# Performance work log

Measured on AMD Instinct MI355X. Metric: run time of the kernel, lower is better.

## Reference

```python
import jax, jax.numpy as jnp
import numpy as np
import math

B, S, D = 1, 2048, 2048
NQ, NKV = 32, 8
HD = D // NQ            # 64
NREP = NQ // NKV        # 4
EPS = 1e-6


def _rope_tables(seq_len, head_dim, theta=10000.0):
    half = head_dim // 2
    inv_freq = 1.0 / (theta ** (np.arange(0, half, dtype=np.float32) / half))
    t = np.arange(seq_len, dtype=np.float32)
    freqs = np.outer(t, inv_freq)  # [S, half]
    return jnp.asarray(np.cos(freqs)), jnp.asarray(np.sin(freqs))


def _rmsnorm(x, g, eps=EPS):
    denom = jnp.sqrt(jnp.mean(x * x, axis=-1, keepdims=True) + eps)
    return x / denom * g


def _rope(x, cos, sin):
    # x: [B, S, H, HD]; cos/sin: [S, HD//2]
    half = x.shape[-1] // 2
    x1, x2 = x[..., :half], x[..., half:]
    c = cos[None, :, None, :]
    s = sin[None, :, None, :]
    return jnp.concatenate([x1 * c - x2 * s, x1 * s + x2 * c], axis=-1)


def setup_inputs() -> dict:
    key = jax.random.key(0)
    ks = jax.random.split(key, 6)
    scale = 1.0 / math.sqrt(D)
    x = jax.random.normal(ks[0], (B, S, D), dtype=jnp.float32)
    Wq = jax.random.normal(ks[1], (D, NQ * HD), dtype=jnp.float32) * scale
    Wk = jax.random.normal(ks[2], (D, NKV * HD), dtype=jnp.float32) * scale
    Wv = jax.random.normal(ks[3], (D, NKV * HD), dtype=jnp.float32) * scale
    Wo = jax.random.normal(ks[4], (NQ * HD, D), dtype=jnp.float32) * scale
    g_q = jnp.ones((HD,), dtype=jnp.float32)
    g_k = jnp.ones((HD,), dtype=jnp.float32)
    cos, sin = _rope_tables(S, HD)
    return {"x": x, "cos": cos, "sin": sin, "g_q": g_q, "g_k": g_k,
            "Wq": Wq, "Wk": Wk, "Wv": Wv, "Wo": Wo}


def reference(x, cos, sin, g_q, g_k, Wq, Wk, Wv, Wo):
    bs, seq, _ = x.shape
    Q = (x @ Wq).reshape(bs, seq, NQ, HD)
    K = (x @ Wk).reshape(bs, seq, NKV, HD)
    V = (x @ Wv).reshape(bs, seq, NKV, HD)
    Q = _rope(_rmsnorm(Q, g_q), cos, sin)
    K = _rope(_rmsnorm(K, g_k), cos, sin)
    # GQA: repeat_interleave KV heads to match Q heads
    K = jnp.repeat(K, NREP, axis=2)  # [B,S,NQ,HD]
    V = jnp.repeat(V, NREP, axis=2)
    # scores: [B, H, S, S]
    scores = jnp.einsum('bshd,bthd->bhst', Q, K) / math.sqrt(HD)
    mask = jnp.triu(jnp.ones((seq, seq), dtype=bool), k=1)
    scores = jnp.where(mask, -jnp.inf, scores)
    attn = jax.nn.softmax(scores, axis=-1)
    out = jnp.einsum('bhst,bthd->bshd', attn, V).reshape(bs, seq, NQ * HD)
    return out @ Wo
```

## Files before the change

### kernel.cpp

```cpp
#include <hip/hip_runtime.h>
#include <hip/hip_bf16.h>
#include <math.h>

#define S 2048
#define D 2048
#define NQ 32
#define NKV 8
#define HD 64
#define HALF 32
#define NREP 4
#define QKV_N 3072
#define KCOL 2048
#define VCOL 2560

typedef unsigned short ushort_t;
typedef __attribute__((ext_vector_type(8))) short bf16x8;
typedef __attribute__((ext_vector_type(4))) float f32x4;
typedef float f4 __attribute__((ext_vector_type(4)));

__device__ __forceinline__ ushort_t f2bf(float f) {
    __hip_bfloat16 h = __float2bfloat16(f);
    return *reinterpret_cast<ushort_t*>(&h);
}
__device__ __forceinline__ float bf2f(ushort_t u) {
    __hip_bfloat16 h = *reinterpret_cast<__hip_bfloat16*>(&u);
    return __bfloat162float(h);
}

__device__ __forceinline__ void load_lds16(const ushort_t* g, ushort_t* l) {
    __builtin_amdgcn_global_load_lds(
        (const __attribute__((address_space(1))) unsigned int*)g,
        (__attribute__((address_space(3))) unsigned int*)l,
        16, 0, 0);
}

__global__ __launch_bounds__(256) void convert_bf16(const float* __restrict__ src,
                                                    ushort_t* __restrict__ dst, int n) {
    int i = (blockIdx.x * 256 + threadIdx.x) * 4;
    if (i + 3 < n) {
        f4 v = *(const f4*)&src[i];
        dst[i + 0] = f2bf(v[0]);
        dst[i + 1] = f2bf(v[1]);
        dst[i + 2] = f2bf(v[2]);
        dst[i + 3] = f2bf(v[3]);
    }
}

__global__ __launch_bounds__(256) void zero_f32(f4* __restrict__ p, int n4) {
    int i = blockIdx.x * 256 + threadIdx.x;
    if (i < n4) p[i] = (f4){0.f, 0.f, 0.f, 0.f};
}

__global__ __launch_bounds__(256) void transpose_w(const float* __restrict__ src,
                                                   ushort_t* __restrict__ dst,
                                                   int Kdim, int N, int pitch, int row_off) {
    __shared__ float tile[32][33];
    const int n0 = blockIdx.x * 32, k0 = blockIdx.y * 32;
    const int tx = threadIdx.x & 31, ty = threadIdx.x >> 5;
    #pragma unroll
    for (int i = 0; i < 32; i += 8)
        tile[ty + i][tx] = src[(size_t)(k0 + ty + i) * N + (n0 + tx)];
    __syncthreads();
    #pragma unroll
    for (int i = 0; i < 32; i += 8)
        dst[(size_t)(row_off + n0 + ty + i) * pitch + (k0 + tx)] = f2bf(tile[tx][ty + i]);
}

__global__ __launch_bounds__(256) void transpose_v(const ushort_t* __restrict__ src,
                                                   ushort_t* __restrict__ dst) {
    __shared__ ushort_t tile[32][33];
    const int s0 = blockIdx.x * 32, d0 = blockIdx.y * 32;
    const int tx = threadIdx.x & 31, ty = threadIdx.x >> 5;
    #pragma unroll
    for (int i = 0; i < 32; i += 8)
        tile[ty + i][tx] = src[(size_t)(s0 + ty + i) * QKV_N + VCOL + d0 + tx];
    __syncthreads();
    #pragma unroll
    for (int i = 0; i < 32; i += 8)
        dst[(size_t)(d0 + ty + i) * S + s0 + tx] = tile[tx][ty + i];
}

template <typename OutT>
__global__ __launch_bounds__(256) void gemm_bt64(const ushort_t* __restrict__ A,
                                                 const ushort_t* __restrict__ BT,
                                                 OutT* __restrict__ C,
                                                 int M, int N, int Kdim) {
    __shared__ ushort_t As[64][32];
    __shared__ ushort_t Bs[128][32];
    const int tid = threadIdx.x;
    const int w = tid >> 6, lane = tid & 63;
    const int r16 = lane & 15, quad = lane >> 4;
    const int wm = (w >> 1) * 32, wn = (w & 1) * 64;
    const int bm = blockIdx.y * 64, bn = blockIdx.x * 128;
    const int sr = lane >> 2;
    const int sc8 = (lane & 3) * 8;

    f32x4 acc[2][4];
    #pragma unroll
    for (int r = 0; r < 2; ++r)
        #pragma unroll
        for (int c = 0; c < 4; ++c) acc[r][c] = (f32x4){0.f, 0.f, 0.f, 0.f};

    for (int k0 = 0; k0 < Kdim; k0 += 32) {
        __syncthreads();
        load_lds16(A + (size_t)(bm + w * 16 + sr) * Kdim + k0 + sc8, &As[w * 16][0]);
        #pragma unroll
        for (int i = 0; i < 2; ++i)
            load_lds16(BT + (size_t)(bn + w * 32 + i * 16 + sr) * Kdim + k0 + sc8,
                       &Bs[w * 32 + i * 16][0]);
        __syncthreads();

        bf16x8 af[2], bfr[4];
        #pragma unroll
        for (int r = 0; r < 2; ++r) af[r]  = *(const bf16x8*)&As[wm + 16 * r + r16][quad * 8];
        #pragma unroll
        for (int c = 0; c < 4; ++c) bfr[c] = *(const bf16x8*)&Bs[wn + 16 * c + r16][quad * 8];
        #pragma unroll
        for (int r = 0; r < 2; ++r)
            #pragma unroll
            for (int c = 0; c < 4; ++c)
                acc[r][c] = __builtin_amdgcn_mfma_f32_16x16x32_bf16(af[r], bfr[c], acc[r][c], 0, 0, 0);
    }

    #pragma unroll
    for (int r = 0; r < 2; ++r)
        #pragma unroll
        for (int c = 0; c < 4; ++c)
            #pragma unroll
            for (int reg = 0; reg < 4; ++reg) {
                int row = bm + wm + 16 * r + quad * 4 + reg;
                int col = bn + wn + 16 * c + r16;
                float v = acc[r][c][reg];
                if constexpr (sizeof(OutT) == 2) C[(size_t)row * N + col] = (OutT)f2bf(v);
                else                             C[(size_t)row * N + col] = (OutT)v;
            }
}

__global__ __launch_bounds__(256) void rmsnorm_rope_b(ushort_t* __restrict__ QKV,
                                                      const float* __restrict__ gq,
                                                      const float* __restrict__ gk,
                                                      const float* __restrict__ cosT,
                                                      const float* __restrict__ sinT) {
    const int s = blockIdx.x;
    const int w = threadIdx.x >> 6;
    const int hh = blockIdx.y * 4 + w;
    const int d = threadIdx.x & 63;
    const float* g;
    int col;
    if (hh < NQ) { g = gq; col = hh * HD; }
    else         { g = gk; col = KCOL + (hh - NQ) * HD; }

    ushort_t* xp = QKV + (size_t)s * QKV_N + col;
    float v = bf2f(xp[d]);
    float ss = v * v;
    #pragma unroll
    for (int off = 32; off > 0; off >>= 1) ss += __shfl_down(ss, off);
    ss = __shfl(ss, 0);
    float inv = rsqrtf(ss * (1.0f / HD) + 1e-6f);
    float xn = v * inv * g[d];

    float other = __shfl(xn, d ^ 32);
    float c = cosT[(size_t)s * HALF + (d & 31)];
    float sn = sinT[(size_t)s * HALF + (d & 31)];
    float outv = (d < HALF) ? (xn * c - other * sn) : (other * sn + xn * c);
    xp[d] = f2bf(outv);
}

__global__ __launch_bounds__(256) void flash_attn_mfma(const ushort_t* __restrict__ QKV,
                                                       const ushort_t* __restrict__ VTg,
                                                       ushort_t* __restrict__ O,
                                                       float* __restrict__ AccBuf,
                                                       float* __restrict__ AccL) {
    __shared__ ushort_t Ks[2][64][64];
    __shared__ ushort_t Vt[2][64][64];
    __shared__ ushort_t Ps[4][16][72];

    const int bx = blockIdx.x;
    int qt, tb, te;
    bool atom;
    if (bx < 16) { qt = 16 + bx; tb = 0; te = 16; atom = true; }
    else         { qt = 47 - bx; atom = (qt >= 16); tb = atom ? 16 : 0; te = qt + 1; }

    const int q0 = qt * 64;
    const int h  = blockIdx.y;
    const int kvh = h >> 2;
    const int tid = threadIdx.x;
    const int w = tid >> 6, lane = tid & 63;
    const int r16 = lane & 15, quad = lane >> 4;
    const int kcol = KCOL + kvh * HD;
    const int vtrow0 = kvh * HD;
    const int rsub = lane >> 3;
    const int jlog = (lane & 7) ^ rsub;
    const int rx = r16 & 7;

    const ushort_t* qrow = QKV + (size_t)(q0 + 16 * w + r16) * QKV_N + h * HD;
    bf16x8 qf0, qf1;
    {
        bf16x8 r0 = *(const bf16x8*)(qrow + quad * 8);
        bf16x8 r1 = *(const bf16x8*)(qrow + quad * 8 + 32);
        #pragma unroll
        for (int j = 0; j < 8; ++j) {
            qf0[j] = (short)f2bf(bf2f((ushort_t)r0[j]) * 0.18033688f);
            qf1[j] = (short)f2bf(bf2f((ushort_t)r1[j]) * 0.18033688f);
        }
    }

    bf16x8 onesf;
    {
        ushort_t ov = (r16 == 0) ? (ushort_t)0x3F80 : (ushort_t)0;
        #pragma unroll
        for (int j = 0; j < 8; ++j) onesf[j] = (short)ov;
    }

    f32x4 accO[4];
    f32x4 accL = (f32x4){0.f, 0.f, 0.f, 0.f};
    #pragma unroll
    for (int c = 0; c < 4; ++c) accO[c] = (f32x4){0.f, 0.f, 0.f, 0.f};

    auto stage = [&](int b, int t0) {
        #pragma unroll
        for (int i = 0; i < 2; ++i) {
            int base = w * 16 + i * 8;
            int row = base + rsub;
            load_lds16(QKV + (size_t)(t0 + row) * QKV_N + kcol + jlog * 8, &Ks[b][base][0]);
            load_lds16(VTg + (size_t)(vtrow0 + row) * S + t0 + jlog * 8, &Vt[b][base][0]);
        }
    };

    stage(tb & 1, tb * 64);

    for (int t = tb; t < te; ++t) {
        __syncthreads();
        if (t + 1 < te) stage((t + 1) & 1, (t + 1) * 64);

        const ushort_t (*K_)[64] = Ks[t & 1];
        const ushort_t (*V_)[64] = Vt[t & 1];
        const bool diag = (t == qt);

        f32x4 sc[4];
        #pragma unroll
        for (int c = 0; c < 4; ++c) {
            bf16x8 kf0 = *(const bf16x8*)&K_[16 * c + r16][(quad ^ rx) * 8];
            bf16x8 kf1 = *(const bf16x8*)&K_[16 * c + r16][((quad + 4) ^ rx) * 8];
            f32x4 z = (f32x4){0.f, 0.f, 0.f, 0.f};
            z = __builtin_amdgcn_mfma_f32_16x16x32_bf16(qf0, kf0, z, 0, 0, 0);
            z = __builtin_amdgcn_mfma_f32_16x16x32_bf16(qf1, kf1, z, 0, 0, 0);
            sc[c] = z;
        }

        #pragma unroll
        for (int c = 0; c < 4; ++c)
            #pragma unroll
            for (int reg = 0; reg < 4; ++reg) {
                float v = sc[c][reg];
                if (diag && (16 * c + r16 > 16 * w + quad * 4 + reg)) v = -INFINITY;
                float p = exp2f(v);
                Ps[w][quad * 4 + reg][16 * c + r16] = f2bf(p);
            }

        bf16x8 pf0 = *(const bf16x8*)&Ps[w][r16][quad * 8];
        bf16x8 pf1 = *(const bf16x8*)&Ps[w][r16][quad * 8 + 32];

        accL = __builtin_amdgcn_mfma_f32_16x16x32_bf16(pf0, onesf, accL, 0, 0, 0);
        accL = __builtin_amdgcn_mfma_f32_16x16x32_bf16(pf1, onesf, accL, 0, 0, 0);

        #pragma unroll
        for (int c = 0; c < 4; ++c) {
            bf16x8 vf0 = *(const bf16x8*)&V_[16 * c + r16][(quad ^ rx) * 8];
            bf16x8 vf1 = *(const bf16x8*)&V_[16 * c + r16][((quad + 4) ^ rx) * 8];
            accO[c] = __builtin_amdgcn_mfma_f32_16x16x32_bf16(pf0, vf0, accO[c], 0, 0, 0);
            accO[c] = __builtin_amdgcn_mfma_f32_16x16x32_bf16(pf1, vf1, accO[c], 0, 0, 0);
        }
    }

    if (!atom) {
        #pragma unroll
        for (int reg = 0; reg < 4; ++reg) {
            float l = __shfl(accL[reg], lane & 48);
            float invl = 1.0f / l;
            int row = q0 + 16 * w + quad * 4 + reg;
            ushort_t* op = O + (size_t)row * D + h * HD;
            #pragma unroll
            for (int c = 0; c < 4; ++c)
                op[16 * c + r16] = f2bf(accO[c][reg] * invl);
        }
    } else {
        const int pair = (qt - 16) * 32 + h;
        float* ab = AccBuf + (size_t)pair * 4096;
        #pragma unroll
        for (int reg = 0; reg < 4; ++reg) {
            int row = 16 * w + quad * 4 + reg;
            #pragma unroll
            for (int c = 0; c < 4; ++c)
                atomicAdd(&ab[row * 64 + 16 * c + r16], accO[c][reg]);
        }
        if (r16 == 0) {
            #pragma unroll
            for (int reg = 0; reg < 4; ++reg)
                atomicAdd(&AccL[pair * 64 + 16 * w + quad * 4 + reg], accL[reg]);
        }
    }
}

__global__ __launch_bounds__(256) void normalize_o(const float* __restrict__ AccBuf,
                                                   const float* __restrict__ AccL,
                                                   ushort_t* __restrict__ O) {
    const int pair = blockIdx.x;
    const int qt = 16 + (pair >> 5);
    const int h  = pair & 31;
    const float* ab = AccBuf + (size_t)pair * 4096;
    const float* lp = AccL + pair * 64;
    for (int i = threadIdx.x; i < 4096; i += 256) {
        int row = i >> 6, d = i & 63;
        O[(size_t)(qt * 64 + row) * D + h * HD + d] = f2bf(ab[i] / lp[row]);
    }
}

extern "C" void kernel_launch(void* const* d_in, const int* in_sizes, int n_in,
                              void* d_out, int out_size, void* d_ws, size_t ws_size,
                              hipStream_t stream) {
    const float* x    = (const float*)d_in[0];
    const float* cosT = (const float*)d_in[1];
    const float* sinT = (const float*)d_in[2];
    const float* g_q  = (const float*)d_in[3];
    const float* g_k  = (const float*)d_in[4];
    const float* Wq   = (const float*)d_in[5];
    const float* Wk   = (const float*)d_in[6];
    const float* Wv   = (const float*)d_in[7];
    const float* Wo   = (const float*)d_in[8];
    float* out = (float*)d_out;

    char* base = (char*)d_ws;
    ushort_t* Xb     = (ushort_t*)base;
    ushort_t* WqkvT  = (ushort_t*)(base + 8388608);
    ushort_t* QKVb   = (ushort_t*)(base + 20971520);
    float*    AccBuf = (float*)(base + 8388608);
    ushort_t* WoT    = (ushort_t*)(base + 8388608);
    ushort_t* VTg    = (ushort_t*)(base + 16777216);
    float*    AccL   = (float*)(base + 18874368);
    ushort_t* Ob     = Xb;

    convert_bf16<<<(S * D) / 1024, 256, 0, stream>>>(x, Xb, S * D);
    transpose_w<<<dim3(2048 / 32, 2048 / 32), 256, 0, stream>>>(Wq, WqkvT, 2048, 2048, 2048, 0);
    transpose_w<<<dim3(512 / 32, 2048 / 32), 256, 0, stream>>>(Wk, WqkvT, 2048, 512, 2048, 2048);
    transpose_w<<<dim3(512 / 32, 2048 / 32), 256, 0, stream>>>(Wv, WqkvT, 2048, 512, 2048, 2560);
    gemm_bt64<ushort_t><<<dim3(QKV_N / 128, S / 64), 256, 0, stream>>>(Xb, WqkvT, QKVb, S, QKV_N, D);
    rmsnorm_rope_b<<<dim3(S, 10), 256, 0, stream>>>(QKVb, g_q, g_k, cosT, sinT);
    transpose_v<<<dim3(S / 32, 512 / 32), 256, 0, stream>>>(QKVb, VTg);
    zero_f32<<<(2097152 / 4 + 255) / 256, 256, 0, stream>>>((f4*)AccBuf, 2097152 / 4);
    zero_f32<<<(32768 / 4 + 255) / 256, 256, 0, stream>>>((f4*)AccL, 32768 / 4);
    flash_attn_mfma<<<dim3(48, NQ), 256, 0, stream>>>(QKVb, VTg, Ob, AccBuf, AccL);
    normalize_o<<<512, 256, 0, stream>>>(AccBuf, AccL, Ob);
    transpose_w<<<dim3(2048 / 32, 2048 / 32), 256, 0, stream>>>(Wo, WoT, 2048, 2048, 2048, 0);
    gemm_bt64<float><<<dim3(D / 128, S / 64), 256, 0, stream>>>(Ob, WoT, out, S, D, D);
}
```

Before: 282.1 us.

## Merge prep kernels, retile GEMM to 64x64 with K=64, shrink attention KV tile

Fuses the x conversion and Q/K/V weight transposes into one launch. RMSNorm+RoPE, the V transpose and the Wo transpose now share a single launch, and the two zeroing kernels become one. The GEMM moves to 64x64 output tiles with a K step of 64 and XOR-swizzled LDS. Attention stages 32-key tiles instead of 64, and the accumulation buffer is moved into the output allocation. The aim is to cut launch overhead and raise block counts, at the cost of smaller per-iteration MFMA work and more loop iterations.

```diff
diff --git a/kernel.cpp b/kernel.cpp
--- a/kernel.cpp
+++ b/kernel.cpp
@@ -34,28 +34,29 @@
         16, 0, 0);
 }
 
-__global__ __launch_bounds__(256) void convert_bf16(const float* __restrict__ src,
-                                                    ushort_t* __restrict__ dst, int n) {
-    int i = (blockIdx.x * 256 + threadIdx.x) * 4;
-    if (i + 3 < n) {
-        f4 v = *(const f4*)&src[i];
-        dst[i + 0] = f2bf(v[0]);
-        dst[i + 1] = f2bf(v[1]);
-        dst[i + 2] = f2bf(v[2]);
-        dst[i + 3] = f2bf(v[3]);
-    }
-}
-
-__global__ __launch_bounds__(256) void zero_f32(f4* __restrict__ p, int n4) {
-    int i = blockIdx.x * 256 + threadIdx.x;
-    if (i < n4) p[i] = (f4){0.f, 0.f, 0.f, 0.f};
-}
-
-__global__ __launch_bounds__(256) void transpose_w(const float* __restrict__ src,
-                                                   ushort_t* __restrict__ dst,
-                                                   int Kdim, int N, int pitch, int row_off) {
+__global__ __launch_bounds__(256) void prep_all(const float* __restrict__ x,
+                                                ushort_t* __restrict__ Xb,
+                                                const float* __restrict__ Wq,
+                                                const float* __restrict__ Wk,
+                                                const float* __restrict__ Wv,
+                                                ushort_t* __restrict__ WqkvT) {
     __shared__ float tile[32][33];
-    const int n0 = blockIdx.x * 32, k0 = blockIdx.y * 32;
+    const int b = blockIdx.x;
+    if (b < 4096) {
+        int i = (b * 256 + threadIdx.x) * 4;
+        f4 v = *(const f4*)&x[i];
+        Xb[i + 0] = f2bf(v[0]);
+        Xb[i + 1] = f2bf(v[1]);
+        Xb[i + 2] = f2bf(v[2]);
+        Xb[i + 3] = f2bf(v[3]);
+        return;
+    }
+    const float* src; int N, row_off, t;
+    if (b < 8192)      { src = Wq; N = 2048; row_off = 0;    t = b - 4096; }
+    else if (b < 9216) { src = Wk; N = 512;  row_off = 2048; t = b - 8192; }
+    else               { src = Wv; N = 512;  row_off = 2560; t = b - 9216; }
+    const int ntn = N / 32;
+    const int n0 = (t % ntn) * 32, k0 = (t / ntn) * 32;
     const int tx = threadIdx.x & 31, ty = threadIdx.x >> 5;
     #pragma unroll
     for (int i = 0; i < 32; i += 8)
@@ -63,69 +64,62 @@
     __syncthreads();
     #pragma unroll
     for (int i = 0; i < 32; i += 8)
-        dst[(size_t)(row_off + n0 + ty + i) * pitch + (k0 + tx)] = f2bf(tile[tx][ty + i]);
-}
-
-__global__ __launch_bounds__(256) void transpose_v(const ushort_t* __restrict__ src,
-                                                   ushort_t* __restrict__ dst) {
-    __shared__ ushort_t tile[32][33];
-    const int s0 = blockIdx.x * 32, d0 = blockIdx.y * 32;
-    const int tx = threadIdx.x & 31, ty = threadIdx.x >> 5;
-    #pragma unroll
-    for (int i = 0; i < 32; i += 8)
-        tile[ty + i][tx] = src[(size_t)(s0 + ty + i) * QKV_N + VCOL + d0 + tx];
-    __syncthreads();
-    #pragma unroll
-    for (int i = 0; i < 32; i += 8)
-        dst[(size_t)(d0 + ty + i) * S + s0 + tx] = tile[tx][ty + i];
+        WqkvT[(size_t)(row_off + n0 + ty + i) * 2048 + (k0 + tx)] = f2bf(tile[tx][ty + i]);
 }
 
 template <typename OutT>
-__global__ __launch_bounds__(256) void gemm_bt64(const ushort_t* __restrict__ A,
-                                                 const ushort_t* __restrict__ BT,
-                                                 OutT* __restrict__ C,
-                                                 int M, int N, int Kdim) {
-    __shared__ ushort_t As[64][32];
-    __shared__ ushort_t Bs[128][32];
+__global__ __launch_bounds__(256) void gemm64(const ushort_t* __restrict__ A,
+                                              const ushort_t* __restrict__ BT,
+                                              OutT* __restrict__ C,
+                                              int M, int N, int Kdim) {
+    __shared__ ushort_t As[64][64];
+    __shared__ ushort_t Bs[64][64];
     const int tid = threadIdx.x;
     const int w = tid >> 6, lane = tid & 63;
     const int r16 = lane & 15, quad = lane >> 4;
-    const int wm = (w >> 1) * 32, wn = (w & 1) * 64;
-    const int bm = blockIdx.y * 64, bn = blockIdx.x * 128;
-    const int sr = lane >> 2;
-    const int sc8 = (lane & 3) * 8;
-
-    f32x4 acc[2][4];
+    const int wm = (w >> 1) * 32, wn = (w & 1) * 32;
+    const int bm = blockIdx.y * 64, bn = blockIdx.x * 64;
+    const int srow = lane >> 3;
+    const int jl = (lane & 7) ^ srow;
+    const int rx = r16 & 7;
+
+    f32x4 acc[2][2];
     #pragma unroll
     for (int r = 0; r < 2; ++r)
         #pragma unroll
-        for (int c = 0; c < 4; ++c) acc[r][c] = (f32x4){0.f, 0.f, 0.f, 0.f};
-
-    for (int k0 = 0; k0 < Kdim; k0 += 32) {
+        for (int c = 0; c < 2; ++c) acc[r][c] = (f32x4){0.f, 0.f, 0.f, 0.f};
+
+    for (int k0 = 0; k0 < Kdim; k0 += 64) {
         __syncthreads();
-        load_lds16(A + (size_t)(bm + w * 16 + sr) * Kdim + k0 + sc8, &As[w * 16][0]);
-        #pragma unroll
-        for (int i = 0; i < 2; ++i)
-            load_lds16(BT + (size_t)(bn + w * 32 + i * 16 + sr) * Kdim + k0 + sc8,
-                       &Bs[w * 32 + i * 16][0]);
+        #pragma unroll
+        for (int i = 0; i < 2; ++i) {
+            int rbase = w * 16 + i * 8;
+            load_lds16(A  + (size_t)(bm + rbase + srow) * Kdim + k0 + jl * 8, &As[rbase][0]);
+            load_lds16(BT + (size_t)(bn + rbase + srow) * Kdim + k0 + jl * 8, &Bs[rbase][0]);
+        }
         __syncthreads();
 
-        bf16x8 af[2], bfr[4];
-        #pragma unroll
-        for (int r = 0; r < 2; ++r) af[r]  = *(const bf16x8*)&As[wm + 16 * r + r16][quad * 8];
-        #pragma unroll
-        for (int c = 0; c < 4; ++c) bfr[c] = *(const bf16x8*)&Bs[wn + 16 * c + r16][quad * 8];
-        #pragma unroll
-        for (int r = 0; r < 2; ++r)
-            #pragma unroll
-            for (int c = 0; c < 4; ++c)
-                acc[r][c] = __builtin_amdgcn_mfma_f32_16x16x32_bf16(af[r], bfr[c], acc[r][c], 0, 0, 0);
+        #pragma unroll
+        for (int h = 0; h < 2; ++h) {
+            bf16x8 af[2], bfr[2];
+            #pragma unroll
+            for (int r = 0; r < 2; ++r)
+                af[r]  = *(const bf16x8*)&As[wm + 16 * r + r16][((quad + 4 * h) ^ rx) * 8];
+            #pragma unroll
+            for (int c = 0; c < 2; ++c)
+                bfr[c] = *(const bf16x8*)&Bs[wn + 16 * c + r16][((quad + 4 * h) ^ rx) * 8];
+            #pragma unroll
+            for (int r = 0; r < 2; ++r)
+                #pragma unroll
+                for (int c = 0; c < 2; ++c)
+                    acc[r][c] = __builtin_amdgcn_mfma_f32_16x16x32_bf16(af[r], bfr[c], acc[r][c], 0, 0, 0);
+        }
     }
 
     #pragma unroll
     for (int r = 0; r < 2; ++r)
         #pragma unroll
-        for (int c = 0; c < 4; ++c)
+        for (int c = 0; c < 2; ++c)
             #pragma unroll
             for (int reg = 0; reg < 4; ++reg) {
                 int row = bm + wm + 16 * r + quad * 4 + reg;
@@ -136,34 +130,73 @@
             }
 }
 
-__global__ __launch_bounds__(256) void rmsnorm_rope_b(ushort_t* __restrict__ QKV,
-                                                      const float* __restrict__ gq,
-                                                      const float* __restrict__ gk,
-                                                      const float* __restrict__ cosT,
-                                                      const float* __restrict__ sinT) {
-    const int s = blockIdx.x;
-    const int w = threadIdx.x >> 6;
-    const int hh = blockIdx.y * 4 + w;
-    const int d = threadIdx.x & 63;
-    const float* g;
-    int col;
-    if (hh < NQ) { g = gq; col = hh * HD; }
-    else         { g = gk; col = KCOL + (hh - NQ) * HD; }
-
-    ushort_t* xp = QKV + (size_t)s * QKV_N + col;
-    float v = bf2f(xp[d]);
-    float ss = v * v;
-    #pragma unroll
-    for (int off = 32; off > 0; off >>= 1) ss += __shfl_down(ss, off);
-    ss = __shfl(ss, 0);
-    float inv = rsqrtf(ss * (1.0f / HD) + 1e-6f);
-    float xn = v * inv * g[d];
-
-    float other = __shfl(xn, d ^ 32);
-    float c = cosT[(size_t)s * HALF + (d & 31)];
-    float sn = sinT[(size_t)s * HALF + (d & 31)];
-    float outv = (d < HALF) ? (xn * c - other * sn) : (other * sn + xn * c);
-    xp[d] = f2bf(outv);
+__global__ __launch_bounds__(256) void rms_rope_vwo(ushort_t* __restrict__ QKV,
+                                                    const float* __restrict__ gq,
+                                                    const float* __restrict__ gk,
+                                                    const float* __restrict__ cosT,
+                                                    const float* __restrict__ sinT,
+                                                    ushort_t* __restrict__ VTg,
+                                                    const float* __restrict__ Wo,
+                                                    ushort_t* __restrict__ WoT) {
+    const int y = blockIdx.y, xb = blockIdx.x;
+    if (y < 10) {
+        const int s = xb;
+        const int w = threadIdx.x >> 6;
+        const int hh = y * 4 + w;
+        const int d = threadIdx.x & 63;
+        const float* g;
+        int col;
+        if (hh < NQ) { g = gq; col = hh * HD; }
+        else         { g = gk; col = KCOL + (hh - NQ) * HD; }
+        ushort_t* xp = QKV + (size_t)s * QKV_N + col;
+        float v = bf2f(xp[d]);
+        float ss = v * v;
+        #pragma unroll
+        for (int off = 32; off > 0; off >>= 1) ss += __shfl_down(ss, off);
+        ss = __shfl(ss, 0);
+        float inv = rsqrtf(ss * (1.0f / HD) + 1e-6f);
+        float xn = v * inv * g[d];
+        float other = __shfl(xn, d ^ 32);
+        float c = cosT[(size_t)s * HALF + (d & 31)];
+        float sn = sinT[(size_t)s * HALF + (d & 31)];
+        float outv = (d < HALF) ? (xn * c - other * sn) : (other * sn + xn * c);
+        xp[d] = f2bf(outv);
+        return;
+    }
+    const int tx = threadIdx.x & 31, ty = threadIdx.x >> 5;
+    if (y == 10 && xb < 1024) {
+        __shared__ ushort_t vt[32][33];
+        const int s0 = (xb & 63) * 32, d0 = (xb >> 6) * 32;
+        #pragma unroll
+        for (int i = 0; i < 32; i += 8)
+            vt[ty + i][tx] = QKV[(size_t)(s0 + ty + i) * QKV_N + VCOL + d0 + tx];
+        __syncthreads();
+        #pragma unroll
+        for (int i = 0; i < 32; i += 8)
+            VTg[(size_t)(d0 + ty + i) * S + s0 + tx] = vt[tx][ty + i];
+        return;
+    }
+    int idx;
+    if (y == 10)      idx = xb - 1024;
+    else if (y == 11) idx = 1024 + xb;
+    else              idx = 3072 + xb;
+    if (idx < 0 || idx >= 4096) return;
+    __shared__ float wt[32][33];
+    const int n0 = (idx & 63) * 32, k0 = (idx >> 6) * 32;
+    #pragma unroll
+    for (int i = 0; i < 32; i += 8)
+        wt[ty + i][tx] = Wo[(size_t)(k0 + ty + i) * 2048 + (n0 + tx)];
+    __syncthreads();
+    #pragma unroll
+    for (int i = 0; i < 32; i += 8)
+        WoT[(size_t)(n0 + ty + i) * 2048 + (k0 + tx)] = f2bf(wt[tx][ty + i]);
+}
+
+__global__ __launch_bounds__(256) void zero_acc(f4* __restrict__ AccBuf4,
+                                                f4* __restrict__ AccL4) {
+    int i = blockIdx.x * 256 + threadIdx.x;
+    if (i < 524288) AccBuf4[i] = (f4){0.f, 0.f, 0.f, 0.f};
+    else if (i < 532480) AccL4[i - 524288] = (f4){0.f, 0.f, 0.f, 0.f};
 }
 
 __global__ __launch_bounds__(256) void flash_attn_mfma(const ushort_t* __restrict__ QKV,
@@ -171,15 +204,15 @@
                                                        ushort_t* __restrict__ O,
                                                        float* __restrict__ AccBuf,
                                                        float* __restrict__ AccL) {
-    __shared__ ushort_t Ks[2][64][64];
-    __shared__ ushort_t Vt[2][64][64];
-    __shared__ ushort_t Ps[4][16][72];
+    __shared__ ushort_t Ks[2][32][64];
+    __shared__ ushort_t Vt[2][64][32];
+    __shared__ ushort_t Ps[4][16][40];
 
     const int bx = blockIdx.x;
     int qt, tb, te;
     bool atom;
-    if (bx < 16) { qt = 16 + bx; tb = 0; te = 16; atom = true; }
-    else         { qt = 47 - bx; atom = (qt >= 16); tb = atom ? 16 : 0; te = qt + 1; }
+    if (bx < 16) { qt = 16 + bx; tb = 0; te = 32; atom = true; }
+    else         { qt = 47 - bx; atom = (qt >= 16); tb = atom ? 32 : 0; te = 2 * qt + 2; }
 
     const int q0 = qt * 64;
     const int h  = blockIdx.y;
@@ -189,9 +222,12 @@
     const int r16 = lane & 15, quad = lane >> 4;
     const int kcol = KCOL + kvh * HD;
     const int vtrow0 = kvh * HD;
-    const int rsub = lane >> 3;
-    const int jlog = (lane & 7) ^ rsub;
+    const int krow = lane >> 3;
+    const int jl = (lane & 7) ^ krow;
+    const int vrow = lane >> 2;
+    const int jv = (lane & 3) ^ (vrow & 3);
     const int rx = r16 & 7;
+    const int rx3 = r16 & 3;
 
     const ushort_t* qrow = QKV + (size_t)(q0 + 16 * w + r16) * QKV_N + h * HD;
     bf16x8 qf0, qf1;
@@ -217,29 +253,28 @@
     #pragma unroll
     for (int c = 0; c < 4; ++c) accO[c] = (f32x4){0.f, 0.f, 0.f, 0.f};
 
-    auto stage = [&](int b, int t0) {
-        #pragma unroll
-        for (int i = 0; i < 2; ++i) {
-            int base = w * 16 + i * 8;
-            int row = base + rsub;
-            load_lds16(QKV + (size_t)(t0 + row) * QKV_N + kcol + jlog * 8, &Ks[b][base][0]);
-            load_lds16(VTg + (size_t)(vtrow0 + row) * S + t0 + jlog * 8, &Vt[b][base][0]);
-        }
+    auto stage = [&](int b, int t) {
+        const int kb = t * 32;
+        load_lds16(QKV + (size_t)(kb + w * 8 + krow) * QKV_N + kcol + jl * 8,
+                   &Ks[b][w * 8][0]);
+        load_lds16(VTg + (size_t)(vtrow0 + w * 16 + vrow) * S + kb + jv * 8,
+                   &Vt[b][w * 16][0]);
     };
 
-    stage(tb & 1, tb * 64);
+    stage(tb & 1, tb);
 
     for (int t = tb; t < te; ++t) {
         __syncthreads();
-        if (t + 1 < te) stage((t + 1) & 1, (t + 1) * 64);
+        if (t + 1 < te) stage((t + 1) & 1, t + 1);
 
         const ushort_t (*K_)[64] = Ks[t & 1];
-        const ushort_t (*V_)[64] = Vt[t & 1];
-        const bool diag = (t == qt);
-
-        f32x4 sc[4];
-        #pragma unroll
-        for (int c = 0; c < 4; ++c) {
+        const ushort_t (*V_)[32] = Vt[t & 1];
+        const int rel = t * 32 - q0;
+        const bool maskt = (rel >= 0);
+
+        f32x4 sc[2];
+        #pragma unroll
+        for (int c = 0; c < 2; ++c) {
             bf16x8 kf0 = *(const bf16x8*)&K_[16 * c + r16][(quad ^ rx) * 8];
             bf16x8 kf1 = *(const bf16x8*)&K_[16 * c + r16][((quad + 4) ^ rx) * 8];
             f32x4 z = (f32x4){0.f, 0.f, 0.f, 0.f};
@@ -249,27 +284,21 @@
         }
 
         #pragma unroll
-        for (int c = 0; c < 4; ++c)
+        for (int c = 0; c < 2; ++c)
             #pragma unroll
             for (int reg = 0; reg < 4; ++reg) {
                 float v = sc[c][reg];
-                if (diag && (16 * c + r16 > 16 * w + quad * 4 + reg)) v = -INFINITY;
-                float p = exp2f(v);
-                Ps[w][quad * 4 + reg][16 * c + r16] = f2bf(p);
+                if (maskt && (rel + 16 * c + r16 > 16 * w + quad * 4 + reg)) v = -INFINITY;
+                Ps[w][quad * 4 + reg][16 * c + r16] = f2bf(exp2f(v));
             }
 
-        bf16x8 pf0 = *(const bf16x8*)&Ps[w][r16][quad * 8];
-        bf16x8 pf1 = *(const bf16x8*)&Ps[w][r16][quad * 8 + 32];
-
-        accL = __builtin_amdgcn_mfma_f32_16x16x32_bf16(pf0, onesf, accL, 0, 0, 0);
-        accL = __builtin_amdgcn_mfma_f32_16x16x32_bf16(pf1, onesf, accL, 0, 0, 0);
-
+        bf16x8 pf = *(const bf16x8*)&Ps[w][r16][quad * 8];
+
+        accL = __builtin_amdgcn_mfma_f32_16x16x32_bf16(pf, onesf, accL, 0, 0, 0);
         #pragma unroll
         for (int c = 0; c < 4; ++c) {
-            bf16x8 vf0 = *(const bf16x8*)&V_[16 * c + r16][(quad ^ rx) * 8];
-            bf16x8 vf1 = *(const bf16x8*)&V_[16 * c + r16][((quad + 4) ^ rx) * 8];
-            accO[c] = __builtin_amdgcn_mfma_f32_16x16x32_bf16(pf0, vf0, accO[c], 0, 0, 0);
-            accO[c] = __builtin_amdgcn_mfma_f32_16x16x32_bf16(pf1, vf1, accO[c], 0, 0, 0);
+            bf16x8 vf = *(const bf16x8*)&V_[16 * c + r16][(quad ^ rx3) * 8];
+            accO[c] = __builtin_amdgcn_mfma_f32_16x16x32_bf16(pf, vf, accO[c], 0, 0, 0);
         }
     }
 
@@ -331,26 +360,20 @@
     float* out = (float*)d_out;
 
     char* base = (char*)d_ws;
-    ushort_t* Xb     = (ushort_t*)base;
-    ushort_t* WqkvT  = (ushort_t*)(base + 8388608);
-    ushort_t* QKVb   = (ushort_t*)(base + 20971520);
-    float*    AccBuf = (float*)(base + 8388608);
-    ushort_t* WoT    = (ushort_t*)(base + 8388608);
-    ushort_t* VTg    = (ushort_t*)(base + 16777216);
-    float*    AccL   = (float*)(base + 18874368);
-    ushort_t* Ob     = Xb;
-
-    convert_bf16<<<(S * D) / 1024, 256, 0, stream>>>(x, Xb, S * D);
-    transpose_w<<<dim3(2048 / 32, 2048 / 32), 256, 0, stream>>>(Wq, WqkvT, 2048, 2048, 2048, 0);
-    transpose_w<<<dim3(512 / 32, 2048 / 32), 256, 0, stream>>>(Wk, WqkvT, 2048, 512, 2048, 2048);
-    transpose_w<<<dim3(512 / 32, 2048 / 32), 256, 0, stream>>>(Wv, WqkvT, 2048, 512, 2048, 2560);
-    gemm_bt64<ushort_t><<<dim3(QKV_N / 128, S / 64), 256, 0, stream>>>(Xb, WqkvT, QKVb, S, QKV_N, D);
-    rmsnorm_rope_b<<<dim3(S, 10), 256, 0, stream>>>(QKVb, g_q, g_k, cosT, sinT);
-    transpose_v<<<dim3(S / 32, 512 / 32), 256, 0, stream>>>(QKVb, VTg);
-    zero_f32<<<(2097152 / 4 + 255) / 256, 256, 0, stream>>>((f4*)AccBuf, 2097152 / 4);
-    zero_f32<<<(32768 / 4 + 255) / 256, 256, 0, stream>>>((f4*)AccL, 32768 / 4);
+    ushort_t* Xb    = (ushort_t*)base;
+    ushort_t* WqkvT = (ushort_t*)(base + 8388608);
+    ushort_t* QKVb  = (ushort_t*)(base + 20971520);
+    ushort_t* WoT   = (ushort_t*)(base + 8388608);
+    ushort_t* VTg   = (ushort_t*)(base + 16777216);
+    float*    AccL  = (float*)(base + 18874368);
+    float*    AccBuf = (float*)d_out;
+    ushort_t* Ob    = Xb;
+
+    prep_all<<<10240, 256, 0, stream>>>(x, Xb, Wq, Wk, Wv, WqkvT);
+    gemm64<ushort_t><<<dim3(QKV_N / 64, S / 64), 256, 0, stream>>>(Xb, WqkvT, QKVb, S, QKV_N, D);
+    rms_rope_vwo<<<dim3(2048, 13), 256, 0, stream>>>(QKVb, g_q, g_k, cosT, sinT, VTg, Wo, WoT);
+    zero_acc<<<2080, 256, 0, stream>>>((f4*)AccBuf, (f4*)AccL);
     flash_attn_mfma<<<dim3(48, NQ), 256, 0, stream>>>(QKVb, VTg, Ob, AccBuf, AccL);
     normalize_o<<<512, 256, 0, stream>>>(AccBuf, AccL, Ob);
-    transpose_w<<<dim3(2048 / 32, 2048 / 32), 256, 0, stream>>>(Wo, WoT, 2048, 2048, 2048, 0);
-    gemm_bt64<float><<<dim3(D / 128, S / 64), 256, 0, stream>>>(Ob, WoT, out, S, D, D);
-}
+    gemm64<float><<<dim3(D / 64, S / 64), 256, 0, stream>>>(Ob, WoT, out, S, D, D);
+}
```

After: 257.5 us. 1.1x faster.
